# Performance work log

Measured on AMD Instinct MI355X. Metric: run time of the kernel, lower is better.

Reference implementation:

```python
import jax, jax.numpy as jnp
import numpy as np

N, E, D = 50000, 800000, 128
LN_EPS = 1e-5


def setup_inputs() -> dict:
    key = jax.random.key(0)
    ks = jax.random.split(key, 6)
    return {
        "x": jax.random.normal(ks[0], (N, D), dtype=jnp.float32),
        "edge_index": jax.random.randint(ks[1], (2, E), 0, N, dtype=jnp.int64),
        "edge_weight": jax.random.uniform(ks[2], (E,), dtype=jnp.float32),
        "lin_w": jax.random.normal(ks[3], (D, D), dtype=jnp.float32) * (1.0 / np.sqrt(D)),
        "lin_b": jax.random.normal(ks[4], (D,), dtype=jnp.float32) * 0.02,
        "ln_gamma": jnp.ones((D,), dtype=jnp.float32),
        "ln_beta": jnp.zeros((D,), dtype=jnp.float32),
    }


def reference(x, edge_index, edge_weight, lin_w, lin_b, ln_gamma, ln_beta):
    n = x.shape[0]
    src, dst = edge_index[0], edge_index[1]
    # degree (by dst), symmetric-ish normalization with +1 smoothing
    deg = jax.ops.segment_sum(jnp.ones(dst.shape, x.dtype), dst, num_segments=n)
    dis = jax.lax.rsqrt(deg + 1.0)  # (N,)
    # gather -> scale -> scatter-add
    scale = (edge_weight * dis[src])[:, None]          # (E,1)
    msg = x[src] * scale                               # (E,D)
    agg = jax.ops.segment_sum(msg, dst, num_segments=n)  # (N,D)
    agg = agg * dis[:, None] + x                       # residual
    # dense tail: Linear -> GELU (exact, matches torch F.gelu) -> LayerNorm
    h = jax.nn.gelu(agg @ lin_w.T + lin_b, approximate=False)
    mu = jnp.mean(h, axis=-1, keepdims=True)
    var = jnp.mean(jnp.square(h - mu), axis=-1, keepdims=True)
    return (h - mu) * jax.lax.rsqrt(var + LN_EPS) * ln_gamma + ln_beta
```

## Files before the change

kernel.cpp:

```cpp
#include <hip/hip_runtime.h>
#include <math.h>

#define D 128
#define CAP 48
#define LDS_STRIDE 136
#define CHUNKS 256
#define BCAP 2048
#define BSH 11

typedef __bf16  bf16x8 __attribute__((ext_vector_type(8)));
typedef float   f32x4  __attribute__((ext_vector_type(4)));

static __device__ __forceinline__ unsigned short f2bf(float f) {
    unsigned int u = __float_as_uint(f);
    u = (u + 0x7fffu + ((u >> 16) & 1u)) >> 16;
    return (unsigned short)u;
}
static __device__ __forceinline__ unsigned int pack2bf(float lo, float hi) {
    return (unsigned int)f2bf(lo) | ((unsigned int)f2bf(hi) << 16);
}
static __device__ __forceinline__ float bflo(unsigned int u) { return __uint_as_float(u << 16); }
static __device__ __forceinline__ float bfhi(unsigned int u) { return __uint_as_float(u & 0xffff0000u); }

__global__ __launch_bounds__(1024) void k_scatter_direct(const int* __restrict__ src,
                                                         const int* __restrict__ dst,
                                                         const float* __restrict__ ew,
                                                         int* __restrict__ gcnt,
                                                         unsigned int* __restrict__ rec,
                                                         int e_count, int cs, int nbk) {
    __shared__ int hist[1024];
    __shared__ int cur[1024];
    int tid = threadIdx.x, c = blockIdx.x;
    for (int b = tid; b < nbk; b += 1024) hist[b] = 0;
    __syncthreads();
    int lo = c * cs, hi = min(lo + cs, e_count);
    for (int i = lo + tid; i < hi; i += 1024) atomicAdd(&hist[dst[i] >> 6], 1);
    __syncthreads();
    for (int b = tid; b < nbk; b += 1024) {
        int h = hist[b];
        int base = h ? atomicAdd(&gcnt[b], h) : 0;
        cur[b] = (b << BSH) + base;
    }
    __syncthreads();
    for (int i = lo + tid; i < hi; i += 1024) {
        int d = dst[i];
        unsigned int q = (unsigned int)(ew[i] * 1023.0f + 0.5f);
        unsigned int r = (q << 22) | ((unsigned int)(d & 63) << 16) | (unsigned int)src[i];
        int pos = atomicAdd(&cur[d >> 6], 1);
        rec[pos] = r;
    }
}

__global__ __launch_bounds__(256) void k_sortcast(unsigned int* __restrict__ rec,
                                                  const int* __restrict__ gcnt,
                                                  const float* __restrict__ x,
                                                  unsigned short* __restrict__ xs,
                                                  int* __restrict__ deg,
                                                  int* __restrict__ offs, int n) {
    __shared__ int hist[64], curs[64];
    __shared__ unsigned int srt[BCAP];
    int tid = threadIdx.x, b = blockIdx.x;
    int base = b << BSH;
    int cnt = min(gcnt[b], BCAP);
    if (tid < 64) hist[tid] = 0;
    __syncthreads();
    for (int i = tid; i < cnt; i += 256) atomicAdd(&hist[(rec[base + i] >> 16) & 63], 1);
    __syncthreads();
    if (tid < 64) {
        int dg = hist[tid];
        int incl = dg;
        #pragma unroll
        for (int off = 1; off < 64; off <<= 1) {
            int t = __shfl_up(incl, off);
            if (tid >= off) incl += t;
        }
        int excl = incl - dg;
        curs[tid] = excl;
        int node = b * 64 + tid;
        if (node < n) {
            deg[node]  = dg;
            offs[node] = base + excl;
        }
    }
    __syncthreads();
    for (int i = tid; i < cnt; i += 256) {
        unsigned int r = rec[base + i];
        int rank = atomicAdd(&curs[(r >> 16) & 63], 1);
        srt[rank] = r;
    }
    __syncthreads();
    for (int i = tid; i < cnt; i += 256) rec[base + i] = srt[i];

    for (int i4 = tid; i4 < 64 * 32; i4 += 256) {
        int lm   = i4 >> 5;
        int node = b * 64 + lm;
        if (node < n) {
            float dd = rsqrtf((float)hist[lm] + 1.0f);
            float4 v = ((const float4*)x)[(size_t)node * 32 + (i4 & 31)];
            ushort4 u;
            u.x = f2bf(v.x * dd); u.y = f2bf(v.y * dd);
            u.z = f2bf(v.z * dd); u.w = f2bf(v.w * dd);
            ((ushort4*)xs)[(size_t)node * 32 + (i4 & 31)] = u;
        }
    }
}


__global__ __launch_bounds__(256) void k_gather_csr(const unsigned short* __restrict__ xs,
                                                    const float* __restrict__ x,
                                                    const int* __restrict__ offs,
                                                    const int* __restrict__ deg,
                                                    const unsigned int* __restrict__ rec,
                                                    unsigned short* __restrict__ aggbf, int n) {
    int node = (int)((blockIdx.x * blockDim.x + threadIdx.x) >> 6);
    int lane = threadIdx.x & 63;
    if (node >= n) return;
    int beg = offs[node];
    int dgv = deg[node];
    int end = beg + dgv;
    const float wq = 1.0f / 1023.0f;
    float ax = 0.f, ay = 0.f;

    int e = beg;
    for (; e + 3 < end; e += 4) {
        unsigned int r0 = rec[e + 0], r1 = rec[e + 1], r2 = rec[e + 2], r3 = rec[e + 3];
        unsigned int u0 = ((const unsigned int*)(xs + (size_t)(r0 & 0xffffu) * D))[lane];
        unsigned int u1 = ((const unsigned int*)(xs + (size_t)(r1 & 0xffffu) * D))[lane];
        unsigned int u2 = ((const unsigned int*)(xs + (size_t)(r2 & 0xffffu) * D))[lane];
        unsigned int u3 = ((const unsigned int*)(xs + (size_t)(r3 & 0xffffu) * D))[lane];
        float w0 = (float)(r0 >> 22) * wq;
        float w1 = (float)(r1 >> 22) * wq;
        float w2 = (float)(r2 >> 22) * wq;
        float w3 = (float)(r3 >> 22) * wq;
        ax += w0 * bflo(u0); ay += w0 * bfhi(u0);
        ax += w1 * bflo(u1); ay += w1 * bfhi(u1);
        ax += w2 * bflo(u2); ay += w2 * bfhi(u2);
        ax += w3 * bflo(u3); ay += w3 * bfhi(u3);
    }
    for (; e < end; ++e) {
        unsigned int r = rec[e];
        unsigned int u = ((const unsigned int*)(xs + (size_t)(r & 0xffffu) * D))[lane];
        float w = (float)(r >> 22) * wq;
        ax += w * bflo(u); ay += w * bfhi(u);
    }

    float dd = rsqrtf((float)dgv + 1.0f);
    float2 xv = ((const float2*)(x + (size_t)node * D))[lane];
    ((unsigned int*)(aggbf + (size_t)node * D))[lane] = pack2bf(ax * dd + xv.x, ay * dd + xv.y);
}


__global__ __launch_bounds__(1024) void k_tail_bf(const unsigned short* __restrict__ aggbf,
                                                  float* __restrict__ out,
                                                  const float* __restrict__ W,
                                                  const float* __restrict__ bias,
                                                  const float* __restrict__ gamma,
                                                  const float* __restrict__ beta, int n) {
    __shared__ unsigned short Bl[128 * LDS_STRIDE];

    int tid  = threadIdx.x;
    int lane = tid & 63;
    int wave = tid >> 6;
    int n16  = lane & 15;
    int quad = lane >> 4;

    #pragma unroll
    for (int it = 0; it < 4; ++it) {
        int idx4 = it * 1024 + tid;
        float4 w4 = ((const float4*)W)[idx4];
        int t  = idx4 >> 5;
        int k4 = (idx4 & 31) << 2;
        ushort4 u;
        u.x = f2bf(w4.x); u.y = f2bf(w4.y); u.z = f2bf(w4.z); u.w = f2bf(w4.w);
        *(ushort4*)&Bl[t * LDS_STRIDE + k4] = u;
    }
    __syncthreads();

    int row0w = blockIdx.x * 256 + wave * 16;
    int arow  = row0w + n16;

    bf16x8 afr[4];
    #pragma unroll
    for (int ko = 0; ko < 4; ++ko)
        afr[ko] = __builtin_bit_cast(bf16x8,
            *(const uint4*)&aggbf[(size_t)arow * D + ko * 32 + quad * 8]);

    f32x4 acc[8];
    #pragma unroll
    for (int nt = 0; nt < 8; ++nt) acc[nt] = (f32x4){0.f, 0.f, 0.f, 0.f};

    #pragma unroll
    for (int nt = 0; nt < 8; ++nt) {
        #pragma unroll
        for (int ko = 0; ko < 4; ++ko) {
            bf16x8 bfr = __builtin_bit_cast(bf16x8,
                *(const uint4*)&Bl[(nt * 16 + n16) * LDS_STRIDE + ko * 32 + quad * 8]);
            acc[nt] = __builtin_amdgcn_mfma_f32_16x16x32_bf16(afr[ko], bfr, acc[nt], 0, 0, 0);
        }
    }

    float bcol[8], gcol[8], betcol[8];
    #pragma unroll
    for (int nt = 0; nt < 8; ++nt) {
        int col = nt * 16 + n16;
        bcol[nt]   = bias[col];
        gcol[nt]   = gamma[col];
        betcol[nt] = beta[col];
    }

    #pragma unroll
    for (int r = 0; r < 4; ++r) {
        float h[8];
        float s1 = 0.f, s2 = 0.f;
        #pragma unroll
        for (int nt = 0; nt < 8; ++nt) {
            float v = acc[nt][r] + bcol[nt];
            v = 0.5f * v * (1.0f + erff(v * 0.70710678118654752f));
            h[nt] = v;
            s1 += v; s2 += v * v;
        }
        #pragma unroll
        for (int mask = 1; mask < 16; mask <<= 1) {
            s1 += __shfl_xor(s1, mask);
            s2 += __shfl_xor(s2, mask);
        }
        float mu  = s1 * (1.0f / 128.0f);
        float var = s2 * (1.0f / 128.0f) - mu * mu;
        float inv = rsqrtf(var + 1e-5f);
        int row = row0w + quad * 4 + r;
        if (row < n) {
            #pragma unroll
            for (int nt = 0; nt < 8; ++nt)
                out[(size_t)row * D + nt * 16 + n16] = (h[nt] - mu) * inv * gcol[nt] + betcol[nt];
        }
    }
}


__global__ __launch_bounds__(256) void k_fillp8(const int* __restrict__ src,
                                                const int* __restrict__ dst,
                                                const float* __restrict__ ew,
                                                int* __restrict__ cnt,
                                                int2* __restrict__ rec, int e_count) {
    int e = blockIdx.x * blockDim.x + threadIdx.x;
    if (e >= e_count) return;
    int d = dst[e];
    int pos = atomicAdd(&cnt[d], 1);
    if (pos < CAP)
        rec[(size_t)d * CAP + pos] = make_int2(src[e], __float_as_int(ew[e]));
}

__global__ __launch_bounds__(256) void k_gatherp_f32(const float* __restrict__ x,
                                                     const int* __restrict__ cnt,
                                                     const int2* __restrict__ rec,
                                                     float* __restrict__ agg, int n) {
    int node = (int)((blockIdx.x * blockDim.x + threadIdx.x) >> 6);
    int lane = threadIdx.x & 63;
    if (node >= n) return;
    int c = cnt[node];
    int m = min(c, CAP);
    size_t base = (size_t)node * CAP;
    float ax = 0.f, ay = 0.f;
    for (int i = 0; i < m; ++i) {
        int2 p = rec[base + i];
        float w = __int_as_float(p.y) * rsqrtf((float)cnt[p.x] + 1.0f);
        float2 v = ((const float2*)(x + (size_t)p.x * D))[lane];
        ax += w * v.x; ay += w * v.y;
    }
    float dd = rsqrtf((float)c + 1.0f);
    float2 xv = ((const float2*)(x + (size_t)node * D))[lane];
    float2 o;
    o.x = ax * dd + xv.x;
    o.y = ay * dd + xv.y;
    ((float2*)(agg + (size_t)node * D))[lane] = o;
}

__global__ __launch_bounds__(256) void k_tail_mfma(float* __restrict__ io,
                                                   const float* __restrict__ W,
                                                   const float* __restrict__ bias,
                                                   const float* __restrict__ gamma,
                                                   const float* __restrict__ beta, int n) {
    __shared__ unsigned short Bl[128 * LDS_STRIDE];
    __shared__ unsigned short Al[4][16 * LDS_STRIDE];

    int tid  = threadIdx.x;
    int lane = tid & 63;
    int wave = tid >> 6;
    int n16  = lane & 15;
    int quad = lane >> 4;

    #pragma unroll
    for (int it = 0; it < 16; ++it) {
        int idx4 = it * 256 + tid;
        float4 w4 = ((const float4*)W)[idx4];
        int t  = idx4 >> 5;
        int k4 = (idx4 & 31) << 2;
        ushort4 u;
        u.x = f2bf(w4.x); u.y = f2bf(w4.y); u.z = f2bf(w4.z); u.w = f2bf(w4.w);
        *(ushort4*)&Bl[t * LDS_STRIDE + k4] = u;
    }
    int row0w = blockIdx.x * 64 + wave * 16;
    #pragma unroll
    for (int j = 0; j < 8; ++j) {
        int idx4 = j * 64 + lane;
        int m  = idx4 >> 5;
        int k4 = (idx4 & 31) << 2;
        int row = row0w + m;
        float4 a4 = make_float4(0.f, 0.f, 0.f, 0.f);
        if (row < n) a4 = ((const float4*)(io + (size_t)row * D))[idx4 & 31];
        ushort4 u;
        u.x = f2bf(a4.x); u.y = f2bf(a4.y); u.z = f2bf(a4.z); u.w = f2bf(a4.w);
        *(ushort4*)&Al[wave][m * LDS_STRIDE + k4] = u;
    }
    __syncthreads();

    bf16x8 afr[4];
    #pragma unroll
    for (int ko = 0; ko < 4; ++ko)
        afr[ko] = __builtin_bit_cast(bf16x8,
            *(const uint4*)&Al[wave][n16 * LDS_STRIDE + ko * 32 + quad * 8]);

    f32x4 acc[8];
    #pragma unroll
    for (int nt = 0; nt < 8; ++nt) acc[nt] = (f32x4){0.f, 0.f, 0.f, 0.f};

    #pragma unroll
    for (int nt = 0; nt < 8; ++nt) {
        #pragma unroll
        for (int ko = 0; ko < 4; ++ko) {
            bf16x8 bfr = __builtin_bit_cast(bf16x8,
                *(const uint4*)&Bl[(nt * 16 + n16) * LDS_STRIDE + ko * 32 + quad * 8]);
            acc[nt] = __builtin_amdgcn_mfma_f32_16x16x32_bf16(afr[ko], bfr, acc[nt], 0, 0, 0);
        }
    }

    float bcol[8], gcol[8], betcol[8];
    #pragma unroll
    for (int nt = 0; nt < 8; ++nt) {
        int col = nt * 16 + n16;
        bcol[nt]   = bias[col];
        gcol[nt]   = gamma[col];
        betcol[nt] = beta[col];
    }

    #pragma unroll
    for (int r = 0; r < 4; ++r) {
        float h[8];
        float s1 = 0.f, s2 = 0.f;
        #pragma unroll
        for (int nt = 0; nt < 8; ++nt) {
            float v = acc[nt][r] + bcol[nt];
            v = 0.5f * v * (1.0f + erff(v * 0.70710678118654752f));
            h[nt] = v;
            s1 += v; s2 += v * v;
        }
        #pragma unroll
        for (int mask = 1; mask < 16; mask <<= 1) {
            s1 += __shfl_xor(s1, mask);
            s2 += __shfl_xor(s2, mask);
        }
        float mu  = s1 * (1.0f / 128.0f);
        float var = s2 * (1.0f / 128.0f) - mu * mu;
        float inv = rsqrtf(var + 1e-5f);
        int row = row0w + quad * 4 + r;
        if (row < n) {
            #pragma unroll
            for (int nt = 0; nt < 8; ++nt)
                io[(size_t)row * D + nt * 16 + n16] = (h[nt] - mu) * inv * gcol[nt] + betcol[nt];
        }
    }
}


extern "C" void kernel_launch(void* const* d_in, const int* in_sizes, int n_in,
                              void* d_out, int out_size, void* d_ws, size_t ws_size,
                              hipStream_t stream) {
    const float* x    = (const float*)d_in[0];
    const int*   ei   = (const int*)d_in[1];
    const float* ew   = (const float*)d_in[2];
    const float* linw = (const float*)d_in[3];
    const float* linb = (const float*)d_in[4];
    const float* lng  = (const float*)d_in[5];
    const float* lnb  = (const float*)d_in[6];
    float* out = (float*)d_out;

    int n = in_sizes[0] / D;
    int e = in_sizes[1] / 2;
    const int* src = ei;
    const int* dst = ei + e;

    int nbk = (n + 63) / 64;
    int cs  = (e + CHUNKS - 1) / CHUNKS;
    int gb  = (n + 3) / 4;
    int tb  = (n + 255) / 256;

    char* wsp = (char*)d_ws;
    size_t off = 0;
    auto alloc = [&](size_t bytes) { char* p = wsp + off; off = (off + bytes + 255) & ~(size_t)255; return p; };
    int*            gcnt  = (int*)alloc((size_t)nbk * 4);
    unsigned int*   rec   = (unsigned int*)alloc((size_t)nbk * BCAP * 4);
    int*            deg   = (int*)alloc((size_t)n * 4);
    int*            offs  = (int*)alloc((size_t)n * 4);
    unsigned short* xs    = (unsigned short*)alloc((size_t)n * D * 2);
    unsigned short* aggbf = (unsigned short*)alloc(((size_t)n + 256) * D * 2);
    bool big = (off <= ws_size) && (n <= 65535) && (nbk <= 1024)
               && ((size_t)e <= (size_t)nbk * (BCAP / 2));

    if (big) {
        hipMemsetAsync(gcnt, 0, (size_t)nbk * 4, stream);
        k_scatter_direct<<<CHUNKS, 1024, 0, stream>>>(src, dst, ew, gcnt, rec, e, cs, nbk);
        k_sortcast<<<nbk, 256, 0, stream>>>(rec, gcnt, x, xs, deg, offs, n);
        k_gather_csr<<<gb, 256, 0, stream>>>(xs, x, offs, deg, rec, aggbf, n);
        k_tail_bf<<<tb, 1024, 0, stream>>>(aggbf, out, linw, linb, lng, lnb, n);
    } else {
        size_t off2 = 0;
        auto alloc2 = [&](size_t bytes) { char* p = wsp + off2; off2 = (off2 + bytes + 255) & ~(size_t)255; return p; };
        int*  cnt2 = (int*)alloc2((size_t)n * 4);
        int2* rec8 = (int2*)alloc2((size_t)n * CAP * 8);
        hipMemsetAsync(cnt2, 0, (size_t)n * 4, stream);
        int eb = (e + 255) / 256;
        int tb64 = (n + 63) / 64;
        k_fillp8<<<eb, 256, 0, stream>>>(src, dst, ew, cnt2, rec8, e);
        k_gatherp_f32<<<gb, 256, 0, stream>>>(x, cnt2, rec8, out, n);
        k_tail_mfma<<<tb64, 256, 0, stream>>>(out, linw, linb, lng, lnb, n);
    }
}
```

Before: 167.2 us.

## Fuse bucket sort with CSR gather and compute degree during scatter

Per-node degree is now counted with global atomics in the scatter pass, so the bf16 cast of x becomes its own fully parallel kernel. The per-bucket sort and the neighbor gather are fused into one 1024-thread kernel that keeps the sorted records in LDS, which removes the write-back of sorted records and the offs/deg arrays. The aim is to cut global traffic and one launch. In exchange it adds 800k global atomics on deg, and with only about 782 blocks of 16 waves each, load balance across CUs may suffer.

```diff
diff --git a/kernel.cpp b/kernel.cpp
--- a/kernel.cpp
+++ b/kernel.cpp
@@ -26,6 +26,7 @@
                                                          const int* __restrict__ dst,
                                                          const float* __restrict__ ew,
                                                          int* __restrict__ gcnt,
+                                                         int* __restrict__ deg,
                                                          unsigned int* __restrict__ rec,
                                                          int e_count, int cs, int nbk) {
     __shared__ int hist[1024];
@@ -34,7 +35,11 @@
     for (int b = tid; b < nbk; b += 1024) hist[b] = 0;
     __syncthreads();
     int lo = c * cs, hi = min(lo + cs, e_count);
-    for (int i = lo + tid; i < hi; i += 1024) atomicAdd(&hist[dst[i] >> 6], 1);
+    for (int i = lo + tid; i < hi; i += 1024) {
+        int d = dst[i];
+        atomicAdd(&hist[d >> 6], 1);
+        atomicAdd(&deg[d], 1);
+    }
     __syncthreads();
     for (int b = tid; b < nbk; b += 1024) {
         int h = hist[b];
@@ -51,20 +56,36 @@
     }
 }
 
-__global__ __launch_bounds__(256) void k_sortcast(unsigned int* __restrict__ rec,
-                                                  const int* __restrict__ gcnt,
-                                                  const float* __restrict__ x,
-                                                  unsigned short* __restrict__ xs,
-                                                  int* __restrict__ deg,
-                                                  int* __restrict__ offs, int n) {
-    __shared__ int hist[64], curs[64];
+
+__global__ __launch_bounds__(256) void k_cast(const float* __restrict__ x,
+                                              const int* __restrict__ deg,
+                                              unsigned short* __restrict__ xs, int n) {
+    int i4 = blockIdx.x * 256 + threadIdx.x;
+    int nq = n * (D / 4);
+    if (i4 >= nq) return;
+    int node = i4 >> 5;
+    float dd = rsqrtf((float)deg[node] + 1.0f);
+    float4 v = ((const float4*)x)[i4];
+    ushort4 u;
+    u.x = f2bf(v.x * dd); u.y = f2bf(v.y * dd);
+    u.z = f2bf(v.z * dd); u.w = f2bf(v.w * dd);
+    ((ushort4*)xs)[i4] = u;
+}
+
+__global__ __launch_bounds__(1024, 8) void k_sortgather(const unsigned int* __restrict__ rec,
+                                                        const int* __restrict__ gcnt,
+                                                        const unsigned short* __restrict__ xs,
+                                                        const float* __restrict__ x,
+                                                        unsigned short* __restrict__ aggbf, int n) {
+    __shared__ int hist[64], loffs[64], curs[64];
     __shared__ unsigned int srt[BCAP];
     int tid = threadIdx.x, b = blockIdx.x;
     int base = b << BSH;
     int cnt = min(gcnt[b], BCAP);
+
     if (tid < 64) hist[tid] = 0;
     __syncthreads();
-    for (int i = tid; i < cnt; i += 256) atomicAdd(&hist[(rec[base + i] >> 16) & 63], 1);
+    for (int i = tid; i < cnt; i += 1024) atomicAdd(&hist[(rec[base + i] >> 16) & 63], 1);
     __syncthreads();
     if (tid < 64) {
         int dg = hist[tid];
@@ -75,78 +96,57 @@
             if (tid >= off) incl += t;
         }
         int excl = incl - dg;
-        curs[tid] = excl;
-        int node = b * 64 + tid;
-        if (node < n) {
-            deg[node]  = dg;
-            offs[node] = base + excl;
-        }
-    }
-    __syncthreads();
-    for (int i = tid; i < cnt; i += 256) {
+        loffs[tid] = excl;
+        curs[tid]  = excl;
+    }
+    __syncthreads();
+    for (int i = tid; i < cnt; i += 1024) {
         unsigned int r = rec[base + i];
         int rank = atomicAdd(&curs[(r >> 16) & 63], 1);
         srt[rank] = r;
     }
     __syncthreads();
-    for (int i = tid; i < cnt; i += 256) rec[base + i] = srt[i];
-
-    for (int i4 = tid; i4 < 64 * 32; i4 += 256) {
-        int lm   = i4 >> 5;
+
+    int wave = tid >> 6, lane = tid & 63;
+    const float wq = 1.0f / 1023.0f;
+
+    #pragma unroll 1
+    for (int j = 0; j < 4; ++j) {
+        int lm   = wave * 4 + j;
         int node = b * 64 + lm;
-        if (node < n) {
-            float dd = rsqrtf((float)hist[lm] + 1.0f);
-            float4 v = ((const float4*)x)[(size_t)node * 32 + (i4 & 31)];
-            ushort4 u;
-            u.x = f2bf(v.x * dd); u.y = f2bf(v.y * dd);
-            u.z = f2bf(v.z * dd); u.w = f2bf(v.w * dd);
-            ((ushort4*)xs)[(size_t)node * 32 + (i4 & 31)] = u;
-        }
-    }
-}
-
-
-__global__ __launch_bounds__(256) void k_gather_csr(const unsigned short* __restrict__ xs,
-                                                    const float* __restrict__ x,
-                                                    const int* __restrict__ offs,
-                                                    const int* __restrict__ deg,
-                                                    const unsigned int* __restrict__ rec,
-                                                    unsigned short* __restrict__ aggbf, int n) {
-    int node = (int)((blockIdx.x * blockDim.x + threadIdx.x) >> 6);
-    int lane = threadIdx.x & 63;
-    if (node >= n) return;
-    int beg = offs[node];
-    int dgv = deg[node];
-    int end = beg + dgv;
-    const float wq = 1.0f / 1023.0f;
-    float ax = 0.f, ay = 0.f;
-
-    int e = beg;
-    for (; e + 3 < end; e += 4) {
-        unsigned int r0 = rec[e + 0], r1 = rec[e + 1], r2 = rec[e + 2], r3 = rec[e + 3];
-        unsigned int u0 = ((const unsigned int*)(xs + (size_t)(r0 & 0xffffu) * D))[lane];
-        unsigned int u1 = ((const unsigned int*)(xs + (size_t)(r1 & 0xffffu) * D))[lane];
-        unsigned int u2 = ((const unsigned int*)(xs + (size_t)(r2 & 0xffffu) * D))[lane];
-        unsigned int u3 = ((const unsigned int*)(xs + (size_t)(r3 & 0xffffu) * D))[lane];
-        float w0 = (float)(r0 >> 22) * wq;
-        float w1 = (float)(r1 >> 22) * wq;
-        float w2 = (float)(r2 >> 22) * wq;
-        float w3 = (float)(r3 >> 22) * wq;
-        ax += w0 * bflo(u0); ay += w0 * bfhi(u0);
-        ax += w1 * bflo(u1); ay += w1 * bfhi(u1);
-        ax += w2 * bflo(u2); ay += w2 * bfhi(u2);
-        ax += w3 * bflo(u3); ay += w3 * bfhi(u3);
-    }
-    for (; e < end; ++e) {
-        unsigned int r = rec[e];
-        unsigned int u = ((const unsigned int*)(xs + (size_t)(r & 0xffffu) * D))[lane];
-        float w = (float)(r >> 22) * wq;
-        ax += w * bflo(u); ay += w * bfhi(u);
-    }
-
-    float dd = rsqrtf((float)dgv + 1.0f);
-    float2 xv = ((const float2*)(x + (size_t)node * D))[lane];
-    ((unsigned int*)(aggbf + (size_t)node * D))[lane] = pack2bf(ax * dd + xv.x, ay * dd + xv.y);
+        if (node >= n) continue;
+        int sbeg = loffs[lm];
+        int dcnt = hist[lm];
+        int send = sbeg + dcnt;
+        float ax = 0.f, ay = 0.f;
+
+        int e = sbeg;
+        for (; e + 3 < send; e += 4) {
+            unsigned int r0 = srt[e + 0], r1 = srt[e + 1], r2 = srt[e + 2], r3 = srt[e + 3];
+            unsigned int u0 = ((const unsigned int*)(xs + (size_t)(r0 & 0xffffu) * D))[lane];
+            unsigned int u1 = ((const unsigned int*)(xs + (size_t)(r1 & 0xffffu) * D))[lane];
+            unsigned int u2 = ((const unsigned int*)(xs + (size_t)(r2 & 0xffffu) * D))[lane];
+            unsigned int u3 = ((const unsigned int*)(xs + (size_t)(r3 & 0xffffu) * D))[lane];
+            float w0 = (float)(r0 >> 22) * wq;
+            float w1 = (float)(r1 >> 22) * wq;
+            float w2 = (float)(r2 >> 22) * wq;
+            float w3 = (float)(r3 >> 22) * wq;
+            ax += w0 * bflo(u0); ay += w0 * bfhi(u0);
+            ax += w1 * bflo(u1); ay += w1 * bfhi(u1);
+            ax += w2 * bflo(u2); ay += w2 * bfhi(u2);
+            ax += w3 * bflo(u3); ay += w3 * bfhi(u3);
+        }
+        for (; e < send; ++e) {
+            unsigned int r = srt[e];
+            unsigned int u = ((const unsigned int*)(xs + (size_t)(r & 0xffffu) * D))[lane];
+            float w = (float)(r >> 22) * wq;
+            ax += w * bflo(u); ay += w * bfhi(u);
+        }
+
+        float dd = rsqrtf((float)dcnt + 1.0f);
+        float2 xv = ((const float2*)(x + (size_t)node * D))[lane];
+        ((unsigned int*)(aggbf + (size_t)node * D))[lane] = pack2bf(ax * dd + xv.x, ay * dd + xv.y);
+    }
 }
 
 
@@ -391,26 +391,26 @@
 
     int nbk = (n + 63) / 64;
     int cs  = (e + CHUNKS - 1) / CHUNKS;
-    int gb  = (n + 3) / 4;
+    int cb  = (n * (D / 4) + 255) / 256;
     int tb  = (n + 255) / 256;
 
     char* wsp = (char*)d_ws;
     size_t off = 0;
     auto alloc = [&](size_t bytes) { char* p = wsp + off; off = (off + bytes + 255) & ~(size_t)255; return p; };
     int*            gcnt  = (int*)alloc((size_t)nbk * 4);
+    int*            deg   = (int*)alloc((size_t)n * 4);
     unsigned int*   rec   = (unsigned int*)alloc((size_t)nbk * BCAP * 4);
-    int*            deg   = (int*)alloc((size_t)n * 4);
-    int*            offs  = (int*)alloc((size_t)n * 4);
     unsigned short* xs    = (unsigned short*)alloc((size_t)n * D * 2);
     unsigned short* aggbf = (unsigned short*)alloc(((size_t)n + 256) * D * 2);
     bool big = (off <= ws_size) && (n <= 65535) && (nbk <= 1024)
                && ((size_t)e <= (size_t)nbk * (BCAP / 2));
 
     if (big) {
-        hipMemsetAsync(gcnt, 0, (size_t)nbk * 4, stream);
-        k_scatter_direct<<<CHUNKS, 1024, 0, stream>>>(src, dst, ew, gcnt, rec, e, cs, nbk);
-        k_sortcast<<<nbk, 256, 0, stream>>>(rec, gcnt, x, xs, deg, offs, n);
-        k_gather_csr<<<gb, 256, 0, stream>>>(xs, x, offs, deg, rec, aggbf, n);
+        size_t zspan = (size_t)((char*)deg - (char*)gcnt) + (size_t)n * 4;
+        hipMemsetAsync(gcnt, 0, zspan, stream);
+        k_scatter_direct<<<CHUNKS, 1024, 0, stream>>>(src, dst, ew, gcnt, deg, rec, e, cs, nbk);
+        k_cast<<<cb, 256, 0, stream>>>(x, deg, xs, n);
+        k_sortgather<<<nbk, 1024, 0, stream>>>(rec, gcnt, xs, x, aggbf, n);
         k_tail_bf<<<tb, 1024, 0, stream>>>(aggbf, out, linw, linb, lng, lnb, n);
     } else {
         size_t off2 = 0;
@@ -419,6 +419,7 @@
         int2* rec8 = (int2*)alloc2((size_t)n * CAP * 8);
         hipMemsetAsync(cnt2, 0, (size_t)n * 4, stream);
         int eb = (e + 255) / 256;
+        int gb = (n + 3) / 4;
         int tb64 = (n + 63) / 64;
         k_fillp8<<<eb, 256, 0, stream>>>(src, dst, ew, cnt2, rec8, e);
         k_gatherp_f32<<<gb, 256, 0, stream>>>(x, cnt2, rec8, out, n);
```

After: 186.4 us. +11.5%, slower.
